# Kernel tuning notes

Hardware: AMD Instinct MI355X
Metric: run time of the kernel (lower is better)

## Reference

```python
import jax, jax.numpy as jnp
import numpy as np

NUM_EXPERTS = 16


def setup_inputs() -> dict:
    key = jax.random.key(0)
    g, s, d = 2, 4096, 1024
    input = jax.random.normal(key, (g, s, d), dtype=jnp.float32)
    return {"input": input}


def reference(input):
    g, s, _ = input.shape
    E = NUM_EXPERTS
    assert s % E == 0
    capacity = 2 * s // E
    i = jnp.arange(s)
    expert = i % E          # round-robin expert assignment
    c = i // E              # capacity slot within expert
    # one-hot dispatch tensor [g, s, E, capacity], identical for every group
    output = jnp.zeros((g, s, E, capacity), dtype=input.dtype)
    output = output.at[:, i, expert, c].set(1.0)
    return (0.0, output, output.astype(jnp.bool_))
```

## Files before the change

### kernel.cpp

```cpp
#include <hip/hip_runtime.h>


#define N1   67108864u
#define NTOT 134217729u
#define NQ   33554432u

__global__ void __launch_bounds__(256) rr_gate_fill(float4* __restrict__ out4,
                                                    float* __restrict__ out) {
    const unsigned stride = gridDim.x * blockDim.x;
    for (unsigned q = blockIdx.x * blockDim.x + threadIdx.x; q < NQ; q += stride) {
        const unsigned p0 = q << 2;
        float4 v;
        float vals[4];
#pragma unroll
        for (int k = 0; k < 4; ++k) {
            const unsigned p = p0 + (unsigned)k;
            float val = 0.0f;
            if (p >= 1u) {
                unsigned j = p - 1u;
                if (j >= N1) j -= N1;
                const unsigned off = j & 8191u;
                const unsigned i   = (j >> 13) & 4095u;
                const unsigned hot = ((i & 15u) << 9) | (i >> 4);
                val = (off == hot) ? 1.0f : 0.0f;
            }
            vals[k] = val;
        }
        v.x = vals[0]; v.y = vals[1]; v.z = vals[2]; v.w = vals[3];
        out4[q] = v;
    }
    if (blockIdx.x == 0 && threadIdx.x == 0) {
        out[NTOT - 1u] = 0.0f;
    }
}

extern "C" void kernel_launch(void* const* d_in, const int* in_sizes, int n_in,
                              void* d_out, int out_size, void* d_ws, size_t ws_size,
                              hipStream_t stream) {
    (void)d_in; (void)in_sizes; (void)n_in; (void)d_ws; (void)ws_size; (void)out_size;
    float* out = (float*)d_out;
    dim3 grid(2048), block(256);
    hipLaunchKernelGGL(rr_gate_fill, grid, block, 0, stream, (float4*)out, out);
}
```

Baseline: 112.3 us.

## Zero output with memset and scatter only the one-hot ones

```diff
diff --git a/kernel.cpp b/kernel.cpp
--- a/kernel.cpp
+++ b/kernel.cpp
@@ -3,35 +3,15 @@
 
 #define N1   67108864u
 #define NTOT 134217729u
-#define NQ   33554432u
 
-__global__ void __launch_bounds__(256) rr_gate_fill(float4* __restrict__ out4,
-                                                    float* __restrict__ out) {
-    const unsigned stride = gridDim.x * blockDim.x;
-    for (unsigned q = blockIdx.x * blockDim.x + threadIdx.x; q < NQ; q += stride) {
-        const unsigned p0 = q << 2;
-        float4 v;
-        float vals[4];
-#pragma unroll
-        for (int k = 0; k < 4; ++k) {
-            const unsigned p = p0 + (unsigned)k;
-            float val = 0.0f;
-            if (p >= 1u) {
-                unsigned j = p - 1u;
-                if (j >= N1) j -= N1;
-                const unsigned off = j & 8191u;
-                const unsigned i   = (j >> 13) & 4095u;
-                const unsigned hot = ((i & 15u) << 9) | (i >> 4);
-                val = (off == hot) ? 1.0f : 0.0f;
-            }
-            vals[k] = val;
-        }
-        v.x = vals[0]; v.y = vals[1]; v.z = vals[2]; v.w = vals[3];
-        out4[q] = v;
-    }
-    if (blockIdx.x == 0 && threadIdx.x == 0) {
-        out[NTOT - 1u] = 0.0f;
-    }
+__global__ void __launch_bounds__(256) rr_gate_ones(float* __restrict__ out) {
+    const unsigned tid = blockIdx.x * blockDim.x + threadIdx.x;
+    const unsigned i   = tid & 4095u;
+    const unsigned g   = (tid >> 12) & 1u;
+    const unsigned t   = tid >> 13;
+    const unsigned hot = ((i & 15u) << 9) | (i >> 4);
+    const unsigned p   = 1u + t * N1 + g * 33554432u + i * 8192u + hot;
+    out[p] = 1.0f;
 }
 
 extern "C" void kernel_launch(void* const* d_in, const int* in_sizes, int n_in,
@@ -39,6 +19,6 @@
                               hipStream_t stream) {
     (void)d_in; (void)in_sizes; (void)n_in; (void)d_ws; (void)ws_size; (void)out_size;
     float* out = (float*)d_out;
-    dim3 grid(2048), block(256);
-    hipLaunchKernelGGL(rr_gate_fill, grid, block, 0, stream, (float4*)out, out);
+    hipMemsetAsync(d_out, 0, (size_t)NTOT * sizeof(float), stream);
+    hipLaunchKernelGGL(rr_gate_ones, dim3(64), dim3(256), 0, stream, out);
 }
```

Result: faster. 93.42 us (-16.8%).
